# Kernel optimization log

Hardware: AMD Instinct MI355X
Metric: run time of the kernel (lower is better)

## Reference

```python
import jax, jax.numpy as jnp
import numpy as np

B, N, F_IN, F_OUT = 16, 2048, 512, 512


def setup_inputs() -> dict:
    key = jax.random.key(0)
    k1, k2, k3 = jax.random.split(key, 3)
    x = jax.random.normal(k1, (B, N, F_IN), dtype=jnp.float32)
    adj = jax.random.uniform(k2, (N, N), dtype=jnp.float32)
    # Kaiming uniform fan_out: bound = sqrt(6 / fan_out)
    bound = np.sqrt(6.0 / F_OUT)
    weight = jax.random.uniform(k3, (F_IN, F_OUT), dtype=jnp.float32,
                                minval=-bound, maxval=bound)
    bias = jnp.zeros((F_OUT,), dtype=jnp.float32)
    return {"x": x, "adj": adj, "weight": weight, "bias": bias}


def reference(x, adj, weight, bias):
    # Symmetric degree normalization: D^{-1/2} A D^{-1/2}
    deg = adj.sum(axis=1)                                   # [N]
    deg_inv_sqrt = jnp.where(deg > 0, jax.lax.rsqrt(deg), 0.0)
    # row/column rescale instead of diag matmuls (same math, O(N^2))
    norm_adj = adj * deg_inv_sqrt[:, None] * deg_inv_sqrt[None, :]
    support = jnp.einsum('bni,io->bno', x, weight)          # [B,N,F_OUT]
    output = jnp.einsum('nm,bmo->bno', norm_adj, support)   # [B,N,F_OUT]
    return output + bias
```

## Files before the change

### kernel.cpp

```cpp
#include <hip/hip_runtime.h>
#include <stdint.h>

typedef __attribute__((ext_vector_type(8))) __bf16 bf16x8;
typedef __attribute__((ext_vector_type(4))) float f32x4;
typedef unsigned short u16;

__device__ __forceinline__ u16 f2bf(float f) {
  unsigned u = __builtin_bit_cast(unsigned, f);
  unsigned r = 0x7FFFu + ((u >> 16) & 1u);
  return (u16)((u + r) >> 16);
}

__device__ __forceinline__ void gload16(const void* g, void* l) {
  __builtin_amdgcn_global_load_lds(
      (__attribute__((address_space(1))) void*)(g),
      (__attribute__((address_space(3))) void*)(l),
      16, 0, 0);
}

__global__ void row_deg_k(const float* __restrict__ adj, float* __restrict__ dis, int N) {
  int row = blockIdx.x;
  const float4* a = (const float4*)(adj + (size_t)row * N);
  float s = 0.f;
  for (int j = threadIdx.x; j < N / 4; j += 256) {
    float4 v = a[j];
    s += v.x + v.y + v.z + v.w;
  }
#pragma unroll
  for (int off = 32; off > 0; off >>= 1) s += __shfl_down(s, off, 64);
  __shared__ float wsum[4];
  if ((threadIdx.x & 63) == 0) wsum[threadIdx.x >> 6] = s;
  __syncthreads();
  if (threadIdx.x == 0) {
    float t = wsum[0] + wsum[1] + wsum[2] + wsum[3];
    dis[row] = (t > 0.f) ? (1.0f / sqrtf(t)) : 0.f;
  }
}

__global__ void conv_bf16_k(const float* __restrict__ in, u16* __restrict__ o, int n4) {
  int i = blockIdx.x * 256 + threadIdx.x;
  if (i >= n4) return;
  float4 v = ((const float4*)in)[i];
  ushort4 u;
  u.x = f2bf(v.x); u.y = f2bf(v.y); u.z = f2bf(v.z); u.w = f2bf(v.w);
  ((ushort4*)o)[i] = u;
}

__global__ void conv_wt_k(const float* __restrict__ w, u16* __restrict__ wt) {
  int idx = blockIdx.x * 256 + threadIdx.x;
  int i = idx >> 9, o = idx & 511;
  wt[o * 512 + i] = f2bf(w[idx]);
}

__global__ void make_nadj_k(const float* __restrict__ adj, const float* __restrict__ dis,
                            u16* __restrict__ o, int N) {
  int idx = blockIdx.x * 256 + threadIdx.x;
  int i = idx >> 9;
  int j4 = (idx & 511) * 4;
  float di = dis[i];
  float4 a = ((const float4*)adj)[idx];
  ushort4 u;
  u.x = f2bf(a.x * di * dis[j4 + 0]);
  u.y = f2bf(a.y * di * dis[j4 + 1]);
  u.z = f2bf(a.z * di * dis[j4 + 2]);
  u.w = f2bf(a.w * di * dis[j4 + 3]);
  ((ushort4*)o)[idx] = u;
}

template <int EPI>
__launch_bounds__(512, 2)
__global__ void gemm256_k(const u16* __restrict__ A, int lda,
                          const u16* __restrict__ Bt, int ldb,
                          void* __restrict__ Cv, int ldc,
                          const float* __restrict__ bias, int K,
                          int nMT, int nNT, size_t zBt, size_t zC) {
  __shared__ __align__(16) u16 lds[65536];

  const int tid = threadIdx.x;
  const int lane = tid & 63;
  const int wid = tid >> 6;
  const int wr = wid >> 2;
  const int wc = wid & 3;

  const int flat = blockIdx.x;
  const int wg = (flat & 7) * ((int)gridDim.x >> 3) + (flat >> 3);
  const int m_t = wg % nMT;
  const int rest = wg / nMT;
  const int n_t = rest % nNT;
  const int b = rest / nNT;
  const int rowBase = m_t * 256;
  const int colBase = n_t * 256;
  const u16* Bb = Bt + (size_t)b * zBt;

  const int lr = tid >> 3;
  const int kkl = (tid & 7) * 8;
  const int kswz = kkl ^ (((lr >> 2) & 3) << 4);
  const u16* gA = A + (size_t)(rowBase + lr) * lda + kswz;
  const u16* gB = Bb + (size_t)(colBase + lr) * ldb + kswz;
  u16* lA = lds + lr * 64 + kkl;
  u16* lB = lds + 32768 + lr * 64 + kkl;

  const int fr = lane & 15;
  const int lswz = ((lane >> 2) & 3) << 4;
  const int kp0 = ((lane >> 4) * 8) ^ lswz;
  const int kp1 = (32 + (lane >> 4) * 8) ^ lswz;
  const u16* fA = lds + (wr * 128 + fr) * 64;
  const u16* fB = lds + 32768 + (wc * 64 + fr) * 64;

  f32x4 acc[8][4] = {};
  bf16x8 As0[4], As1[4], Bs0[4], Bs1[4];

  const int NT = K >> 6;

#define STAGE_ALL(d, t)                                                              \
  _Pragma("unroll") for (int r4 = 0; r4 < 4; ++r4) {                                 \
    gload16(gA + (size_t)(r4 * 64) * lda + (size_t)(t) * 64,                         \
            lA + (d) * 16384 + r4 * 4096);                                           \
    gload16(gB + (size_t)(r4 * 64) * ldb + (size_t)(t) * 64,                         \
            lB + (d) * 16384 + r4 * 4096);                                           \
  }

#define RD_A(dst, mh, kh, c)                                                         \
  _Pragma("unroll") for (int m = 0; m < 4; ++m)                                      \
    dst[m] = *(const bf16x8*)(fA + (c) * 16384 + (mh) * 4096 + m * 1024 + kp##kh);

#define RD_B(dst, kh, c)                                                             \
  _Pragma("unroll") for (int n = 0; n < 4; ++n)                                      \
    dst[n] = *(const bf16x8*)(fB + (c) * 16384 + n * 1024 + kp##kh);

#define MFMA_P(mh, A_, B_)                                                           \
  _Pragma("unroll") for (int m = 0; m < 4; ++m)                                      \
    _Pragma("unroll") for (int n = 0; n < 4; ++n)                                    \
      acc[(mh) * 4 + m][n] = __builtin_amdgcn_mfma_f32_16x16x32_bf16(                \
          A_[m], B_[n], acc[(mh) * 4 + m][n], 0, 0, 0);

  STAGE_ALL(0, 0);
  asm volatile("s_waitcnt vmcnt(0)" ::: "memory");
  __builtin_amdgcn_s_barrier();

  for (int t = 0; t < NT; ++t) {
    const int c = t & 1;
    const int cn = c ^ 1;
    const int tn = (t + 1 < NT) ? t + 1 : NT - 1;

    __builtin_amdgcn_sched_barrier(0);
    STAGE_ALL(cn, tn);
    RD_A(As0, 0, 0, c);
    RD_B(Bs0, 0, c);
    __builtin_amdgcn_sched_barrier(0);

    RD_A(As1, 1, 0, c);
    MFMA_P(0, As0, Bs0);
    __builtin_amdgcn_sched_barrier(0);

    RD_A(As0, 0, 1, c);
    RD_B(Bs1, 1, c);
    MFMA_P(1, As1, Bs0);
    __builtin_amdgcn_sched_barrier(0);

    RD_A(As1, 1, 1, c);
    MFMA_P(0, As0, Bs1);
    __builtin_amdgcn_sched_barrier(0);

    MFMA_P(1, As1, Bs1);
    __builtin_amdgcn_sched_barrier(0);

    asm volatile("s_waitcnt vmcnt(0)" ::: "memory");
    __builtin_amdgcn_sched_barrier(0);
    __builtin_amdgcn_s_barrier();
  }

  if (EPI == 0) {
    u16* C = (u16*)Cv;
#pragma unroll
    for (int am = 0; am < 8; ++am) {
      const int r = rowBase + wr * 128 + (am >> 2) * 64 + (am & 3) * 16 + (lane >> 4) * 4;
#pragma unroll
      for (int n = 0; n < 4; ++n) {
        const int cc = colBase + wc * 64 + n * 16 + (lane & 15);
        ushort4 v;
        v.x = f2bf(acc[am][n][0]);
        v.y = f2bf(acc[am][n][1]);
        v.z = f2bf(acc[am][n][2]);
        v.w = f2bf(acc[am][n][3]);
        *reinterpret_cast<ushort4*>(&C[(size_t)cc * ldc + r]) = v;
      }
    }
  } else {
    float* C = (float*)Cv + (size_t)b * zC;
#pragma unroll
    for (int n = 0; n < 4; ++n) {
      const int cc = colBase + wc * 64 + n * 16 + (lane & 15);
      const float bv = bias[cc];
#pragma unroll
      for (int am = 0; am < 8; ++am) {
        const int r = rowBase + wr * 128 + (am >> 2) * 64 + (am & 3) * 16 + (lane >> 4) * 4;
#pragma unroll
        for (int j = 0; j < 4; ++j)
          C[(size_t)(r + j) * ldc + cc] = acc[am][n][j] + bv;
      }
    }
  }
#undef STAGE_ALL
#undef RD_A
#undef RD_B
#undef MFMA_P
}

extern "C" void kernel_launch(void* const* d_in, const int* in_sizes, int n_in,
                              void* d_out, int out_size, void* d_ws, size_t ws_size,
                              hipStream_t stream) {
  const int B = 16, N = 2048, FIN = 512, FOUT = 512;
  const float* x    = (const float*)d_in[0];
  const float* adj  = (const float*)d_in[1];
  const float* w    = (const float*)d_in[2];
  const float* bias = (const float*)d_in[3];
  float* out = (float*)d_out;
  char* ws = (char*)d_ws;

  float* dis = (float*)ws;
  u16* wt    = (u16*)(ws + 8192);
  u16* nadj  = (u16*)(ws + 532480);
  u16* xb    = (u16*)(ws + 8921088);
  u16* st    = (u16*)(ws + 42475520);

  row_deg_k<<<N, 256, 0, stream>>>(adj, dis, N);
  conv_bf16_k<<<(B * N * FIN / 4 + 255) / 256, 256, 0, stream>>>(x, xb, B * N * FIN / 4);
  conv_wt_k<<<(FIN * FOUT) / 256, 256, 0, stream>>>(w, wt);
  make_nadj_k<<<(N * N / 4) / 256, 256, 0, stream>>>(adj, dis, nadj, N);

  gemm256_k<0><<<dim3(256), 512, 0, stream>>>(
      xb, FIN, wt, FIN, st, B * N, nullptr, FIN, 128, 2, 0, 0);

  gemm256_k<1><<<dim3(256), 512, 0, stream>>>(
      nadj, N, st, B * N, out, FOUT, bias, N, 8, 2,
      (size_t)N, (size_t)N * FOUT);
}
```

Before: 126.4 us.

## Software-pipeline LDS fragment reads across k-tiles, change swizzle, add MFMA setprio

Changes the LDS XOR swizzle to an 8-way pattern based on row index, meant to reduce bank conflicts on fragment reads. The main loop is restructured so the first A/B fragments of the next k-tile are read from LDS before the last MFMA group of the current tile, with the wait and barrier moved earlier. B fragment reads are split into halves, and s_setprio is raised around the MFMA groups. The intent is to hide LDS latency behind MFMA work; it adds a second barrier per iteration and more register pressure.

```diff
diff --git a/kernel.cpp b/kernel.cpp
--- a/kernel.cpp
+++ b/kernel.cpp
@@ -94,16 +94,16 @@
 
   const int lr = tid >> 3;
   const int kkl = (tid & 7) * 8;
-  const int kswz = kkl ^ (((lr >> 2) & 3) << 4);
+  const int kswz = kkl ^ ((lr & 7) << 3);
   const u16* gA = A + (size_t)(rowBase + lr) * lda + kswz;
   const u16* gB = Bb + (size_t)(colBase + lr) * ldb + kswz;
   u16* lA = lds + lr * 64 + kkl;
   u16* lB = lds + 32768 + lr * 64 + kkl;
 
   const int fr = lane & 15;
-  const int lswz = ((lane >> 2) & 3) << 4;
-  const int kp0 = ((lane >> 4) * 8) ^ lswz;
-  const int kp1 = (32 + (lane >> 4) * 8) ^ lswz;
+  const int rswz = (lane & 7) << 3;
+  const int kp0 = ((lane >> 4) * 8) ^ rswz;
+  const int kp1 = (32 | ((lane >> 4) * 8)) ^ rswz;
   const u16* fA = lds + (wr * 128 + fr) * 64;
   const u16* fB = lds + 32768 + (wc * 64 + fr) * 64;
 
@@ -120,23 +120,33 @@
             lB + (d) * 16384 + r4 * 4096);                                           \
   }
 
-#define RD_A(dst, mh, kh, c)                                                         \
+#define RD_A4(dst, mh, kp, c)                                                        \
   _Pragma("unroll") for (int m = 0; m < 4; ++m)                                      \
-    dst[m] = *(const bf16x8*)(fA + (c) * 16384 + (mh) * 4096 + m * 1024 + kp##kh);
-
-#define RD_B(dst, kh, c)                                                             \
+    dst[m] = *(const bf16x8*)(fA + (c) * 16384 + (mh) * 4096 + m * 1024 + (kp));
+
+#define RD_B4(dst, kp, c)                                                            \
   _Pragma("unroll") for (int n = 0; n < 4; ++n)                                      \
-    dst[n] = *(const bf16x8*)(fB + (c) * 16384 + n * 1024 + kp##kh);
+    dst[n] = *(const bf16x8*)(fB + (c) * 16384 + n * 1024 + (kp));
+
+#define RD_B2(dst, nlo, kp, c)                                                       \
+  _Pragma("unroll") for (int n = 0; n < 2; ++n)                                      \
+    dst[(nlo) + n] = *(const bf16x8*)(fB + (c) * 16384 + ((nlo) + n) * 1024 + (kp));
 
 #define MFMA_P(mh, A_, B_)                                                           \
+  __builtin_amdgcn_sched_barrier(0);                                                 \
+  __builtin_amdgcn_s_setprio(1);                                                     \
   _Pragma("unroll") for (int m = 0; m < 4; ++m)                                      \
     _Pragma("unroll") for (int n = 0; n < 4; ++n)                                    \
       acc[(mh) * 4 + m][n] = __builtin_amdgcn_mfma_f32_16x16x32_bf16(                \
-          A_[m], B_[n], acc[(mh) * 4 + m][n], 0, 0, 0);
+          A_[m], B_[n], acc[(mh) * 4 + m][n], 0, 0, 0);                              \
+  __builtin_amdgcn_s_setprio(0);                                                     \
+  __builtin_amdgcn_sched_barrier(0)
 
   STAGE_ALL(0, 0);
   asm volatile("s_waitcnt vmcnt(0)" ::: "memory");
   __builtin_amdgcn_s_barrier();
+  RD_A4(As0, 0, kp0, 0);
+  RD_B4(Bs0, kp0, 0);
 
   for (int t = 0; t < NT; ++t) {
     const int c = t & 1;
@@ -145,30 +155,31 @@
 
     __builtin_amdgcn_sched_barrier(0);
     STAGE_ALL(cn, tn);
-    RD_A(As0, 0, 0, c);
-    RD_B(Bs0, 0, c);
-    __builtin_amdgcn_sched_barrier(0);
-
-    RD_A(As1, 1, 0, c);
+
+    RD_A4(As1, 1, kp0, c);
     MFMA_P(0, As0, Bs0);
-    __builtin_amdgcn_sched_barrier(0);
-
-    RD_A(As0, 0, 1, c);
-    RD_B(Bs1, 1, c);
+
+    RD_A4(As0, 0, kp1, c);
+    RD_B2(Bs1, 0, kp1, c);
     MFMA_P(1, As1, Bs0);
-    __builtin_amdgcn_sched_barrier(0);
-
-    RD_A(As1, 1, 1, c);
+
+    RD_A4(As1, 1, kp1, c);
+    RD_B2(Bs1, 2, kp1, c);
     MFMA_P(0, As0, Bs1);
-    __builtin_amdgcn_sched_barrier(0);
-
+
+    __builtin_amdgcn_sched_barrier(0);
+    asm volatile("s_waitcnt vmcnt(0)" ::: "memory");
+    __builtin_amdgcn_sched_barrier(0);
+    __builtin_amdgcn_s_barrier();
+    __builtin_amdgcn_sched_barrier(0);
+    RD_A4(As0, 0, kp0, cn);
+    RD_B4(Bs0, kp0, cn);
     MFMA_P(1, As1, Bs1);
-    __builtin_amdgcn_sched_barrier(0);
-
-    asm volatile("s_waitcnt vmcnt(0)" ::: "memory");
+
     __builtin_amdgcn_sched_barrier(0);
     __builtin_amdgcn_s_barrier();
   }
+  asm volatile("s_waitcnt vmcnt(0)" ::: "memory");
 
   if (EPI == 0) {
     u16* C = (u16*)Cv;
@@ -202,8 +213,9 @@
     }
   }
 #undef STAGE_ALL
-#undef RD_A
-#undef RD_B
+#undef RD_A4
+#undef RD_B4
+#undef RD_B2
 #undef MFMA_P
 }
 
```

Measured after the change: 125.2 us. Within noise of the previous version (-1.0%).
